# Kernel optimization log

Measured on AMD Instinct MI355X. Metric: run time of the kernel, lower is better.

The kernel has to match this reference:

```python
import jax, jax.numpy as jnp
import numpy as np

B, LQ, LK, D, NH = 16, 1024, 1024, 160, 8
HD = D // NH
EPS = 1e-5


def _ln(x, g, b):
    m = x.mean(-1, keepdims=True)
    v = ((x - m) ** 2).mean(-1, keepdims=True)
    return (x - m) / jnp.sqrt(v + EPS) * g + b


def _heads(x, L):
    # [B,L,D] -> [B,NH,L,HD]
    return x.reshape(B, L, NH, HD).transpose(0, 2, 1, 3)


def _attn(qh, kh, vh, scale):
    logits = jnp.einsum('bhqd,bhkd->bhqk', qh, kh) * scale
    p = jax.nn.softmax(logits, axis=-1)
    o = jnp.einsum('bhqk,bhkd->bhqd', p, vh)
    return o.transpose(0, 2, 1, 3).reshape(B, -1, D)


def setup_inputs() -> dict:
    key = jax.random.key(0)
    ks = jax.random.split(key, 16)
    s = 0.02
    inp = {
        'q': jax.random.normal(ks[0], (B, LQ, D), jnp.float32),
        'kv': jax.random.normal(ks[1], (B, LK, D), jnp.float32),
        'ln1_g': jnp.ones((D,), jnp.float32), 'ln1_b': jnp.zeros((D,), jnp.float32),
        'sa_in_w': jax.random.normal(ks[2], (3 * D, D), jnp.float32) * s,
        'sa_in_b': jnp.zeros((3 * D,), jnp.float32),
        'sa_out_w': jax.random.normal(ks[3], (D, D), jnp.float32) * s,
        'sa_out_b': jnp.zeros((D,), jnp.float32),
        'ln2_g': jnp.ones((D,), jnp.float32), 'ln2_b': jnp.zeros((D,), jnp.float32),
        'lnkv_g': jnp.ones((D,), jnp.float32), 'lnkv_b': jnp.zeros((D,), jnp.float32),
        'ca_qw': jax.random.normal(ks[4], (D, D), jnp.float32) * s,
        'ca_qb': jnp.zeros((D,), jnp.float32),
        'ca_kw': jax.random.normal(ks[5], (D, D), jnp.float32) * s,
        'ca_kb': jnp.zeros((D,), jnp.float32),
        'ca_vw': jax.random.normal(ks[6], (D, D), jnp.float32) * s,
        'ca_vb': jnp.zeros((D,), jnp.float32),
        'ca_ow': jax.random.normal(ks[7], (D, D), jnp.float32) * s,
        'ca_ob': jnp.zeros((D,), jnp.float32),
        'log_tau': jnp.zeros((1,), jnp.float32),
        'lnf_g': jnp.ones((D,), jnp.float32), 'lnf_b': jnp.zeros((D,), jnp.float32),
        'w1': jax.random.normal(ks[8], (4 * D, D), jnp.float32) * s,
        'b1': jnp.zeros((4 * D,), jnp.float32),
        'w2': jax.random.normal(ks[9], (D, 4 * D), jnp.float32) * s,
        'b2': jnp.zeros((D,), jnp.float32),
    }
    return inp


def reference(q, kv, ln1_g, ln1_b, sa_in_w, sa_in_b, sa_out_w, sa_out_b,
              ln2_g, ln2_b, lnkv_g, lnkv_b, ca_qw, ca_qb, ca_kw, ca_kb,
              ca_vw, ca_vb, ca_ow, ca_ob, log_tau, lnf_g, lnf_b,
              w1, b1, w2, b2):
    # --- self-attention (pre-LN), standard 1/sqrt(hd) scale ---
    qn = _ln(q, ln1_g, ln1_b)
    qkv = qn @ sa_in_w.T + sa_in_b  # [B,LQ,3D]
    sq, sk, sv = jnp.split(qkv, 3, axis=-1)
    sa = _attn(_heads(sq, LQ), _heads(sk, LQ), _heads(sv, LQ), HD ** -0.5)
    sa = sa @ sa_out_w.T + sa_out_b
    q = q + sa  # DropPath is identity in eval

    # --- cross-attention with learnable temperature ---
    qn = _ln(q, ln2_g, ln2_b)
    kvn = _ln(kv, lnkv_g, lnkv_b)
    tau = jnp.minimum(jax.nn.softplus(log_tau) + 0.5, 2.0)  # clamp max=2.0
    scale = (HD ** -0.5) / tau[0]
    qh = _heads(qn @ ca_qw.T + ca_qb, LQ)
    kh = _heads(kvn @ ca_kw.T + ca_kb, LK)
    vh = _heads(kvn @ ca_vw.T + ca_vb, LK)
    ca = _attn(qh, kh, vh, scale) @ ca_ow.T + ca_ob
    q = q + ca

    # --- FFN with exact GELU ---
    h = _ln(q, lnf_g, lnf_b) @ w1.T + b1
    h = jax.nn.gelu(h, approximate=False)
    q = q + (h @ w2.T + b2)
    return q
```

## Files before the change

### kernel.cpp

```cpp
#include <hip/hip_runtime.h>
#include <hip/hip_bf16.h>
#include <math.h>

#define LQN 1024
#define LKN 1024
#define NB 16
#define DM 160
#define NHEADS 8
#define HDIM 20

typedef __attribute__((ext_vector_type(8))) short bf16x8;
typedef __attribute__((ext_vector_type(4))) float f32x4;

__device__ __forceinline__ float bf2f(unsigned short h) {
  union { unsigned int u; float f; } c; c.u = ((unsigned int)h) << 16; return c.f;
}
__device__ __forceinline__ unsigned short f2bf(float f) {
  union { float f; unsigned int u; } c; c.f = f;
  unsigned int lsb = (c.u >> 16) & 1u;
  unsigned int r = c.u + 0x7fffu + lsb;
  return (unsigned short)(r >> 16);
}
__device__ __forceinline__ unsigned int cvtpk(float a, float b) {
  unsigned int r;
  asm("v_cvt_pk_bf16_f32 %0, %1, %2" : "=v"(r) : "v"(a), "v"(b));
  return r;
}
__device__ __forceinline__ float ex2(float x) { return __builtin_amdgcn_exp2f(x); }

struct CvtArgs {
  const float* src[8];
  int cum[9];
};

__global__ void init_kernel(uint4* __restrict__ zbase, int nz,
                            uint4* __restrict__ vbase, int nv,
                            const float* __restrict__ b0,
                            const float* __restrict__ b1,
                            const float* __restrict__ b2,
                            float* __restrict__ bcat,
                            CvtArgs a, unsigned short* __restrict__ wdst,
                            const float* __restrict__ x1,
                            const float* __restrict__ g1,
                            const float* __restrict__ bb1,
                            unsigned short* __restrict__ y1,
                            const float* __restrict__ x2,
                            const float* __restrict__ g2,
                            const float* __restrict__ bb2,
                            unsigned short* __restrict__ y2, int rowsPer) {
  int i = blockIdx.x * 256 + threadIdx.x;
  if (i < nz) zbase[i] = make_uint4(0, 0, 0, 0);
  if (i < nv) {
    unsigned int v = ((i & 31) == 20) ? 0x3F803F80u : 0u;
    vbase[i] = make_uint4(v, v, v, v);
  }
  if (i < 480) bcat[i] = (i < 160) ? b0[i] : (i < 320 ? b1[i - 160] : b2[i - 320]);
  if (i < 409600) {
    int s = 0;
#pragma unroll
    for (int t = 0; t < 7; ++t) s += (i >= a.cum[t + 1]) ? 1 : 0;
    wdst[i] = f2bf(a.src[s][i - a.cum[s]]);
  }
  int row = blockIdx.x * 4 + (threadIdx.x >> 6);
  int lane = threadIdx.x & 63;
  const float* x; const float* g; const float* b; unsigned short* y;
  if (row < rowsPer) {
    x = x1 + (size_t)row * DM; g = g1; b = bb1; y = y1 + (size_t)row * DM;
  } else {
    int r2 = row - rowsPer;
    x = x2 + (size_t)r2 * DM; g = g2; b = bb2; y = y2 + (size_t)r2 * DM;
  }
  float a0 = x[lane];
  float a1 = x[lane + 64];
  float a2 = (lane < 32) ? x[lane + 128] : 0.0f;
  float s = a0 + a1 + a2;
#pragma unroll
  for (int m = 1; m < 64; m <<= 1) s += __shfl_xor(s, m);
  float mean = s * (1.0f / DM);
  float d0 = a0 - mean, d1 = a1 - mean, d2 = a2 - mean;
  float vs = d0 * d0 + d1 * d1 + ((lane < 32) ? d2 * d2 : 0.0f);
#pragma unroll
  for (int m = 1; m < 64; m <<= 1) vs += __shfl_xor(vs, m);
  float rstd = rsqrtf(vs * (1.0f / DM) + 1e-5f);
  y[lane]      = f2bf(d0 * rstd * g[lane]      + b[lane]);
  y[lane + 64] = f2bf(d1 * rstd * g[lane + 64] + b[lane + 64]);
  if (lane < 32)
    y[lane + 128] = f2bf(d2 * rstd * g[lane + 128] + b[lane + 128]);
}

template <int EPI, int NCOL>
__global__ __launch_bounds__(256, 2)
void gemm160_kernel(const unsigned short* __restrict__ Aq,
                    const unsigned short* __restrict__ Akv,
                    const unsigned short* __restrict__ W,
                    const float* __restrict__ bias,
                    const float* __restrict__ res,
                    void* __restrict__ outp,
                    unsigned short* __restrict__ Kc,
                    unsigned short* __restrict__ Vc,
                    const float* __restrict__ lng,
                    const float* __restrict__ lnb) {
  __shared__ unsigned short wl[NCOL * 16 * 168];
  int tid = threadIdx.x;
  int lane = tid & 63;
  int w = tid >> 6;
  int y = blockIdx.y;
  const unsigned short* Wb = W + y * (NCOL * 2560);
  for (int idx = tid * 8; idx < NCOL * 2560; idx += 2048) {
    int col = idx / 160, k = idx % 160;
    *(uint4*)(wl + col * 168 + k) = *(const uint4*)(Wb + idx);
  }
  __syncthreads();
  int lr = lane & 15;
  int g = lane >> 4;
  int R0 = blockIdx.x * 64;
  int rbase = R0 + w * 16;
  const unsigned short* A = (EPI == 0 && y > 0) ? Akv : Aq;
  const unsigned short* Ap = A + (size_t)(rbase + lr) * 160 + g * 8;
  const unsigned short* wp = wl + lr * 168 + g * 8;
  f32x4 acc[NCOL];
#pragma unroll
  for (int c = 0; c < NCOL; ++c) acc[c] = (f32x4){0, 0, 0, 0};
#pragma unroll
  for (int k0 = 0; k0 < 160; k0 += 32) {
    bf16x8 a = *(const bf16x8*)(Ap + k0);
#pragma unroll
    for (int c = 0; c < NCOL; ++c) {
      bf16x8 bfr = *(const bf16x8*)(wp + c * 16 * 168 + k0);
      acc[c] = __builtin_amdgcn_mfma_f32_16x16x32_bf16(a, bfr, acc[c], 0, 0, 0);
    }
  }
  if (EPI == 0) {
    if (y == 0) {
      unsigned short* Qp = (unsigned short*)outp;
#pragma unroll
      for (int c = 0; c < NCOL; ++c) {
        int col = c * 16 + lr;
        int h = col / 20, d = col % 20;
        float bc = bias[col];
#pragma unroll
        for (int r = 0; r < 4; ++r) {
          int row = rbase + g * 4 + r;
          Qp[(size_t)row * 256 + h * 32 + d] = f2bf(acc[c][r] + bc);
        }
      }
    } else if (y == 1) {
      int b = R0 >> 10;
#pragma unroll
      for (int c = 0; c < NCOL; ++c) {
        int col = c * 16 + lr;
        int h = col / 20, d = col % 20;
        float bc = bias[160 + col];
        size_t base = ((((size_t)(b * 8 + h)) * 4 + (d >> 3)) * 1024) * 8 + (d & 7);
#pragma unroll
        for (int r = 0; r < 4; ++r) {
          int tok = (rbase + g * 4 + r) & 1023;
          Kc[base + (size_t)tok * 8] = f2bf(acc[c][r] + bc);
        }
      }
    } else {
      int b = R0 >> 10;
      int base64 = R0 & 1023;
      int slotbase = base64 + g * 8 + (w & 1) * 4 + (w >> 1) * 32;
#pragma unroll
      for (int c = 0; c < NCOL; ++c) {
        int col = c * 16 + lr;
        int h = col / 20, d = col % 20;
        float bc = bias[320 + col];
        size_t vb = ((size_t)(b * 8 + h) * 128) * 256 + (size_t)d * 8;
#pragma unroll
        for (int r = 0; r < 4; ++r) {
          int S = slotbase + r;
          Vc[vb + (size_t)(S >> 3) * 256 + (S & 7)] = f2bf(acc[c][r] + bc);
        }
      }
    }
  } else if (EPI == 2) {
    unsigned short* out = (unsigned short*)outp;
#pragma unroll
    for (int c = 0; c < NCOL; ++c) {
      int colg = y * NCOL * 16 + c * 16 + lr;
      float bc = bias[colg];
#pragma unroll
      for (int r = 0; r < 4; ++r) {
        int row = rbase + g * 4 + r;
        float v = acc[c][r] + bc;
        v = 0.5f * v * (1.0f + erff(v * 0.70710678118654752f));
        out[(size_t)row * 640 + colg] = f2bf(v);
      }
    }
  } else {
    float* out = (float*)outp;
#pragma unroll
    for (int c = 0; c < NCOL; ++c) {
      int col = c * 16 + lr;
      float bc = bias[col];
#pragma unroll
      for (int r = 0; r < 4; ++r) {
        int row = rbase + g * 4 + r;
        float v = acc[c][r] + bc + res[(size_t)row * 160 + col];
        acc[c][r] = v;
        out[(size_t)row * 160 + col] = v;
      }
    }
#pragma unroll
    for (int r = 0; r < 4; ++r) {
      float s = 0.0f, sq = 0.0f;
#pragma unroll
      for (int c = 0; c < NCOL; ++c) { s += acc[c][r]; sq += acc[c][r] * acc[c][r]; }
#pragma unroll
      for (int m = 1; m < 16; m <<= 1) { s += __shfl_xor(s, m); sq += __shfl_xor(sq, m); }
      float mean = s * (1.0f / DM);
      float var = sq * (1.0f / DM) - mean * mean;
      float rstd = rsqrtf(var + 1e-5f);
      int row = rbase + g * 4 + r;
#pragma unroll
      for (int c = 0; c < NCOL; ++c) {
        int col = c * 16 + lr;
        Kc[(size_t)row * 160 + col] =
            f2bf((acc[c][r] - mean) * rstd * lng[col] + lnb[col]);
      }
    }
  }
}

template <int K>
__global__ __launch_bounds__(256, 4)
void gemm_kernel(const unsigned short* __restrict__ A,
                 const unsigned short* __restrict__ W,
                 const float* __restrict__ bias,
                 const float* __restrict__ res,
                 float* __restrict__ out, int N) {
  int lane = threadIdx.x & 63;
  int wid = threadIdx.x >> 6;
  int wr = wid >> 1, wc = wid & 1;
  int r0 = blockIdx.x * 64 + wr * 32;
  int c0 = blockIdx.y * 64 + wc * 32;
  if (c0 >= N) return;
  int lr = lane & 15;
  int ko = (lane >> 4) * 8;
  const unsigned short* Ap0 = A + (size_t)(r0 + lr) * K + ko;
  const unsigned short* Ap1 = Ap0 + (size_t)16 * K;
  const unsigned short* Wp0 = W + (size_t)(c0 + lr) * K + ko;
  const unsigned short* Wp1 = Wp0 + (size_t)16 * K;
  f32x4 acc00 = {0, 0, 0, 0}, acc01 = {0, 0, 0, 0};
  f32x4 acc10 = {0, 0, 0, 0}, acc11 = {0, 0, 0, 0};
#pragma unroll
  for (int k = 0; k < K; k += 32) {
    bf16x8 a0 = *(const bf16x8*)(Ap0 + k);
    bf16x8 a1 = *(const bf16x8*)(Ap1 + k);
    bf16x8 b0 = *(const bf16x8*)(Wp0 + k);
    bf16x8 b1 = *(const bf16x8*)(Wp1 + k);
    acc00 = __builtin_amdgcn_mfma_f32_16x16x32_bf16(a0, b0, acc00, 0, 0, 0);
    acc01 = __builtin_amdgcn_mfma_f32_16x16x32_bf16(a0, b1, acc01, 0, 0, 0);
    acc10 = __builtin_amdgcn_mfma_f32_16x16x32_bf16(a1, b0, acc10, 0, 0, 0);
    acc11 = __builtin_amdgcn_mfma_f32_16x16x32_bf16(a1, b1, acc11, 0, 0, 0);
  }
  int cA = c0 + lr, cB = c0 + 16 + lr;
  float bc0 = bias[cA];
  float bc1 = bias[cB];
  int rb = (lane >> 4) * 4;
#pragma unroll
  for (int i = 0; i < 2; ++i) {
    f32x4 aA = i ? acc10 : acc00;
    f32x4 aB = i ? acc11 : acc01;
#pragma unroll
    for (int r = 0; r < 4; ++r) {
      int row = r0 + i * 16 + rb + r;
      out[(size_t)row * N + cA] = aA[r] + bc0 + res[(size_t)row * N + cA];
      out[(size_t)row * N + cB] = aB[r] + bc1 + res[(size_t)row * N + cB];
    }
  }
}

__global__ __launch_bounds__(256, 4)
void attn_kernel(const unsigned short* __restrict__ Qp,
                 const unsigned short* __restrict__ Kc,
                 const unsigned short* __restrict__ Vc,
                 unsigned short* __restrict__ O,
                 const float* __restrict__ tau_ptr,
                 float base_scale) {
  __shared__ unsigned short kbuf[2][4096];
  __shared__ unsigned short vbuf[2][4096];
  int lane = threadIdx.x & 63;
  int wid = threadIdx.x >> 6;
  int bh = blockIdx.x;
  int b = bh >> 3, h = bh & 7;
  int q0 = blockIdx.y * 128 + wid * 32;
  float sc = base_scale;
  if (tau_ptr) {
    float lt = tau_ptr[0];
    float sp = (lt > 20.0f) ? lt : log1pf(expf(lt));
    sc /= fminf(sp + 0.5f, 2.0f);
  }
  float scale = sc * 1.4426950408889634f;
  int lr = lane & 15;
  int g = lane >> 4;
  int ko = g * 8;
  int rb = g * 4;
  const size_t tb = (size_t)b * LQN;
  union { bf16x8 v; unsigned short s[8]; unsigned int u[4]; } fq0, fq1;
  fq0.v = *(const bf16x8*)(Qp + (tb + q0 + lr) * 256 + h * 32 + ko);
  fq1.v = *(const bf16x8*)(Qp + (tb + q0 + 16 + lr) * 256 + h * 32 + ko);
#pragma unroll
  for (int j = 0; j < 4; ++j) {
    fq0.u[j] = cvtpk(bf2f(fq0.s[2 * j]) * scale, bf2f(fq0.s[2 * j + 1]) * scale);
    fq1.u[j] = cvtpk(bf2f(fq1.s[2 * j]) * scale, bf2f(fq1.s[2 * j + 1]) * scale);
  }
  bf16x8 aq0 = fq0.v, aq1 = fq1.v;
  const unsigned short* ksrc = Kc + (((size_t)bh * 4 + wid) * 1024) * 8;
  const unsigned short* vsrc = Vc + (size_t)bh * 32768;
  int sd = wid * 1024 + lane * 8;
  {
    uint4 k0 = *(const uint4*)(ksrc + lane * 8);
    uint4 k1 = *(const uint4*)(ksrc + (64 + lane) * 8);
    uint4 v0 = *(const uint4*)(vsrc + sd);
    uint4 v1 = *(const uint4*)(vsrc + sd + 512);
    *(uint4*)(kbuf[0] + sd) = k0;
    *(uint4*)(kbuf[0] + sd + 512) = k1;
    *(uint4*)(vbuf[0] + sd) = v0;
    *(uint4*)(vbuf[0] + sd + 512) = v1;
  }
  __syncthreads();
  int cur = 0;
  f32x4 o00 = {0, 0, 0, 0}, o01 = {0, 0, 0, 0};
  f32x4 o10 = {0, 0, 0, 0}, o11 = {0, 0, 0, 0};
  const f32x4 zero = {0, 0, 0, 0};

#define ATTN_COMPUTE(KB, VB)                                                   \
  {                                                                            \
    const unsigned short* kp_ = (KB);                                          \
    const unsigned short* vp_ = (VB);                                          \
    bf16x8 ck0 = *(const bf16x8*)(kp_ + g * 1024 + lr * 8);                    \
    bf16x8 ck1 = *(const bf16x8*)(kp_ + g * 1024 + (16 + lr) * 8);             \
    bf16x8 ck2 = *(const bf16x8*)(kp_ + g * 1024 + (32 + lr) * 8);             \
    bf16x8 ck3 = *(const bf16x8*)(kp_ + g * 1024 + (48 + lr) * 8);             \
    __builtin_amdgcn_s_setprio(1);                                             \
    f32x4 s0 = __builtin_amdgcn_mfma_f32_16x16x32_bf16(ck0, aq0, zero, 0, 0, 0);\
    f32x4 s1 = __builtin_amdgcn_mfma_f32_16x16x32_bf16(ck1, aq0, zero, 0, 0, 0);\
    f32x4 s2 = __builtin_amdgcn_mfma_f32_16x16x32_bf16(ck2, aq0, zero, 0, 0, 0);\
    f32x4 s3 = __builtin_amdgcn_mfma_f32_16x16x32_bf16(ck3, aq0, zero, 0, 0, 0);\
    __builtin_amdgcn_s_setprio(0);                                             \
    union { bf16x8 v; unsigned int u[4]; } p1, p2, p3, p4;                     \
    p1.u[0] = cvtpk(ex2(s0[0]), ex2(s0[1]));                                   \
    p1.u[1] = cvtpk(ex2(s0[2]), ex2(s0[3]));                                   \
    p1.u[2] = cvtpk(ex2(s1[0]), ex2(s1[1]));                                   \
    p1.u[3] = cvtpk(ex2(s1[2]), ex2(s1[3]));                                   \
    p2.u[0] = cvtpk(ex2(s2[0]), ex2(s2[1]));                                   \
    p2.u[1] = cvtpk(ex2(s2[2]), ex2(s2[3]));                                   \
    p2.u[2] = cvtpk(ex2(s3[0]), ex2(s3[1]));                                   \
    p2.u[3] = cvtpk(ex2(s3[2]), ex2(s3[3]));                                   \
    __builtin_amdgcn_s_setprio(1);                                             \
    s0 = __builtin_amdgcn_mfma_f32_16x16x32_bf16(ck0, aq1, zero, 0, 0, 0);     \
    s1 = __builtin_amdgcn_mfma_f32_16x16x32_bf16(ck1, aq1, zero, 0, 0, 0);     \
    s2 = __builtin_amdgcn_mfma_f32_16x16x32_bf16(ck2, aq1, zero, 0, 0, 0);     \
    s3 = __builtin_amdgcn_mfma_f32_16x16x32_bf16(ck3, aq1, zero, 0, 0, 0);     \
    __builtin_amdgcn_s_setprio(0);                                             \
    p3.u[0] = cvtpk(ex2(s0[0]), ex2(s0[1]));                                   \
    p3.u[1] = cvtpk(ex2(s0[2]), ex2(s0[3]));                                   \
    p3.u[2] = cvtpk(ex2(s1[0]), ex2(s1[1]));                                   \
    p3.u[3] = cvtpk(ex2(s1[2]), ex2(s1[3]));                                   \
    p4.u[0] = cvtpk(ex2(s2[0]), ex2(s2[1]));                                   \
    p4.u[1] = cvtpk(ex2(s2[2]), ex2(s2[3]));                                   \
    p4.u[2] = cvtpk(ex2(s3[0]), ex2(s3[1]));                                   \
    p4.u[3] = cvtpk(ex2(s3[2]), ex2(s3[3]));                                   \
    bf16x8 w00 = *(const bf16x8*)(vp_ + g * 256 + lr * 8);                     \
    bf16x8 w01 = *(const bf16x8*)(vp_ + (4 + g) * 256 + lr * 8);               \
    bf16x8 w10 = *(const bf16x8*)(vp_ + g * 256 + (16 + lr) * 8);              \
    bf16x8 w11 = *(const bf16x8*)(vp_ + (4 + g) * 256 + (16 + lr) * 8);        \
    __builtin_amdgcn_s_setprio(1);                                             \
    o00 = __builtin_amdgcn_mfma_f32_16x16x32_bf16(p1.v, w00, o00, 0, 0, 0);    \
    o00 = __builtin_amdgcn_mfma_f32_16x16x32_bf16(p2.v, w01, o00, 0, 0, 0);    \
    o01 = __builtin_amdgcn_mfma_f32_16x16x32_bf16(p1.v, w10, o01, 0, 0, 0);    \
    o01 = __builtin_amdgcn_mfma_f32_16x16x32_bf16(p2.v, w11, o01, 0, 0, 0);    \
    o10 = __builtin_amdgcn_mfma_f32_16x16x32_bf16(p3.v, w00, o10, 0, 0, 0);    \
    o10 = __builtin_amdgcn_mfma_f32_16x16x32_bf16(p4.v, w01, o10, 0, 0, 0);    \
    o11 = __builtin_amdgcn_mfma_f32_16x16x32_bf16(p3.v, w10, o11, 0, 0, 0);    \
    o11 = __builtin_amdgcn_mfma_f32_16x16x32_bf16(p4.v, w11, o11, 0, 0, 0);    \
    __builtin_amdgcn_s_setprio(0);                                             \
  }

#pragma unroll 1
  for (int kt = 0; kt < LKN; kt += 128) {
    int ktn = (kt + 128 < LKN) ? kt + 128 : 0;
    uint4 kA0 = *(const uint4*)(ksrc + (ktn + lane) * 8);
    uint4 kA1 = *(const uint4*)(ksrc + (ktn + 64 + lane) * 8);
    uint4 vA0 = *(const uint4*)(vsrc + ktn * 32 + sd);
    uint4 vA1 = *(const uint4*)(vsrc + ktn * 32 + sd + 512);
    ATTN_COMPUTE(kbuf[cur], vbuf[cur])
    *(uint4*)(kbuf[cur ^ 1] + sd) = kA0;
    *(uint4*)(kbuf[cur ^ 1] + sd + 512) = kA1;
    ATTN_COMPUTE(kbuf[cur] + 512, vbuf[cur] + 2048)
    *(uint4*)(vbuf[cur ^ 1] + sd) = vA0;
    *(uint4*)(vbuf[cur ^ 1] + sd + 512) = vA1;
    __syncthreads();
    cur ^= 1;
  }
#undef ATTN_COMPUTE
  unsigned short* ob = O + (tb + q0) * DM + h * HDIM;
  int psl = (lane & 48) + 4;
#pragma unroll
  for (int r = 0; r < 4; ++r) {
    int qr = rb + r;
    float inv0 = 1.0f / __shfl(o01[r], psl, 64);
    ob[(size_t)qr * DM + lr] = f2bf(o00[r] * inv0);
    if (lr < 4) ob[(size_t)qr * DM + 16 + lr] = f2bf(o01[r] * inv0);
    float inv1 = 1.0f / __shfl(o11[r], psl, 64);
    ob[(size_t)(16 + qr) * DM + lr] = f2bf(o10[r] * inv1);
    if (lr < 4) ob[(size_t)(16 + qr) * DM + 16 + lr] = f2bf(o11[r] * inv1);
  }
}

extern "C" void kernel_launch(void* const* d_in, const int* in_sizes, int n_in,
                              void* d_out, int out_size, void* d_ws, size_t ws_size,
                              hipStream_t stream) {
  (void)in_sizes; (void)n_in; (void)out_size; (void)ws_size;
  const float* q        = (const float*)d_in[0];
  const float* kv       = (const float*)d_in[1];
  const float* ln1_g    = (const float*)d_in[2];
  const float* ln1_b    = (const float*)d_in[3];
  const float* sa_in_w  = (const float*)d_in[4];
  const float* sa_in_b  = (const float*)d_in[5];
  const float* sa_out_w = (const float*)d_in[6];
  const float* sa_out_b = (const float*)d_in[7];
  const float* ln2_g    = (const float*)d_in[8];
  const float* ln2_b    = (const float*)d_in[9];
  const float* lnkv_g   = (const float*)d_in[10];
  const float* lnkv_b   = (const float*)d_in[11];
  const float* ca_qw    = (const float*)d_in[12];
  const float* ca_qb    = (const float*)d_in[13];
  const float* ca_kw    = (const float*)d_in[14];
  const float* ca_kb    = (const float*)d_in[15];
  const float* ca_vw    = (const float*)d_in[16];
  const float* ca_vb    = (const float*)d_in[17];
  const float* ca_ow    = (const float*)d_in[18];
  const float* ca_ob    = (const float*)d_in[19];
  const float* log_tau  = (const float*)d_in[20];
  const float* lnf_g    = (const float*)d_in[21];
  const float* lnf_b    = (const float*)d_in[22];
  const float* w1       = (const float*)d_in[23];
  const float* b1       = (const float*)d_in[24];
  const float* w2       = (const float*)d_in[25];
  const float* b2       = (const float*)d_in[26];

  const int M = NB * LQN;
  char* ws = (char*)d_ws;
  unsigned short* wb   = (unsigned short*)(ws);
  float*          bcat = (float*)(ws + 860160);
  unsigned short* qn   = (unsigned short*)(ws + 1048576);
  unsigned short* sqp  = (unsigned short*)(ws + 6291456);
  unsigned short* skc  = (unsigned short*)(ws + 14680064);
  unsigned short* svc  = (unsigned short*)(ws + 23068672);
  unsigned short* attn = (unsigned short*)(ws + 31457280);
  unsigned short* kvn  = (unsigned short*)(ws + 36700160);
  float*          q1   = (float*)(ws + 41943040);
  float*          q2   = (float*)(ws + 52428800);
  unsigned short* hbuf = (unsigned short*)(ws + 6291456);

  unsigned short* b_sa_in  = wb;
  unsigned short* b_sa_out = wb + 76800;
  unsigned short* b_ca_q   = wb + 102400;
  unsigned short* b_ca_o   = wb + 179200;
  unsigned short* b_w1     = wb + 204800;
  unsigned short* b_w2     = wb + 307200;

  dim3 blk(256);
  const float isq = 0.22360679774997896f;

  CvtArgs ca;
  ca.src[0] = sa_in_w;  ca.src[1] = sa_out_w; ca.src[2] = ca_qw; ca.src[3] = ca_kw;
  ca.src[4] = ca_vw;    ca.src[5] = ca_ow;    ca.src[6] = w1;    ca.src[7] = w2;
  int cum[9] = {0, 76800, 102400, 128000, 153600, 179200, 204800, 307200, 409600};
  for (int i = 0; i < 9; ++i) ca.cum[i] = cum[i];
  init_kernel<<<dim3(M / 2), blk, 0, stream>>>(
      (uint4*)(ws + 6291456), 1048576, (uint4*)(ws + 23068672), 524288,
      ca_qb, ca_kb, ca_vb, bcat, ca, wb,
      q, ln1_g, ln1_b, qn, kv, lnkv_g, lnkv_b, kvn, M);

  gemm160_kernel<0, 10><<<dim3(M / 64, 3), blk, 0, stream>>>(
      qn, qn, b_sa_in, sa_in_b, nullptr, sqp, skc, svc, nullptr, nullptr);
  attn_kernel<<<dim3(NB * NHEADS, LQN / 128), blk, 0, stream>>>(sqp, skc, svc, attn, nullptr, isq);
  gemm160_kernel<3, 10><<<dim3(M / 64, 1), blk, 0, stream>>>(
      attn, attn, b_sa_out, sa_out_b, q, q1, qn, nullptr, ln2_g, ln2_b);

  gemm160_kernel<0, 10><<<dim3(M / 64, 3), blk, 0, stream>>>(
      qn, kvn, b_ca_q, bcat, nullptr, sqp, skc, svc, nullptr, nullptr);
  attn_kernel<<<dim3(NB * NHEADS, LQN / 128), blk, 0, stream>>>(sqp, skc, svc, attn, log_tau, isq);
  gemm160_kernel<3, 10><<<dim3(M / 64, 1), blk, 0, stream>>>(
      attn, attn, b_ca_o, ca_ob, q1, q2, qn, nullptr, lnf_g, lnf_b);

  gemm160_kernel<2, 10><<<dim3(M / 64, 4), blk, 0, stream>>>(
      qn, qn, b_w1, b1, nullptr, hbuf, nullptr, nullptr, nullptr, nullptr);
  gemm_kernel<640><<<dim3(M / 64, 3), blk, 0, stream>>>(hbuf, b_w2, b2, q2, (float*)d_out, 160);
}
```

Baseline: 163.8 us.

## Give each wave private K/V LDS tiles to drop block-wide barriers

The attention kernel no longer shares double-buffered K/V tiles across the four waves of a block. Each wave now loads its own copy of every 64-key tile from global memory into a private LDS region, with the next tile prefetched into registers while the current one is computed. This removes the per-iteration __syncthreads so waves can run independently. The cost is four times the global/L2 load traffic per block, twice as many loop iterations, and reliance on in-order LDS access within a wave for the single-buffer overwrite.

```diff
diff --git a/kernel.cpp b/kernel.cpp
--- a/kernel.cpp
+++ b/kernel.cpp
@@ -280,8 +280,8 @@
                  unsigned short* __restrict__ O,
                  const float* __restrict__ tau_ptr,
                  float base_scale) {
-  __shared__ unsigned short kbuf[2][4096];
-  __shared__ unsigned short vbuf[2][4096];
+  __shared__ unsigned short kpriv[4][2048];
+  __shared__ unsigned short vpriv[4][2048];
   int lane = threadIdx.x & 63;
   int wid = threadIdx.x >> 6;
   int bh = blockIdx.x;
@@ -308,95 +308,97 @@
     fq1.u[j] = cvtpk(bf2f(fq1.s[2 * j]) * scale, bf2f(fq1.s[2 * j + 1]) * scale);
   }
   bf16x8 aq0 = fq0.v, aq1 = fq1.v;
-  const unsigned short* ksrc = Kc + (((size_t)bh * 4 + wid) * 1024) * 8;
+  const unsigned short* ksrc = Kc + (size_t)bh * 32768;
   const unsigned short* vsrc = Vc + (size_t)bh * 32768;
-  int sd = wid * 1024 + lane * 8;
-  {
-    uint4 k0 = *(const uint4*)(ksrc + lane * 8);
-    uint4 k1 = *(const uint4*)(ksrc + (64 + lane) * 8);
-    uint4 v0 = *(const uint4*)(vsrc + sd);
-    uint4 v1 = *(const uint4*)(vsrc + sd + 512);
-    *(uint4*)(kbuf[0] + sd) = k0;
-    *(uint4*)(kbuf[0] + sd + 512) = k1;
-    *(uint4*)(vbuf[0] + sd) = v0;
-    *(uint4*)(vbuf[0] + sd + 512) = v1;
-  }
-  __syncthreads();
-  int cur = 0;
+  unsigned short* kw = kpriv[wid];
+  unsigned short* vw = vpriv[wid];
+  int lo = lane * 8;
+  uint4 kr0 = *(const uint4*)(ksrc + lo);
+  uint4 kr1 = *(const uint4*)(ksrc + 8192 + lo);
+  uint4 kr2 = *(const uint4*)(ksrc + 16384 + lo);
+  uint4 kr3 = *(const uint4*)(ksrc + 24576 + lo);
+  uint4 vr0 = *(const uint4*)(vsrc + lo);
+  uint4 vr1 = *(const uint4*)(vsrc + 512 + lo);
+  uint4 vr2 = *(const uint4*)(vsrc + 1024 + lo);
+  uint4 vr3 = *(const uint4*)(vsrc + 1536 + lo);
+  *(uint4*)(kw + lo) = kr0;
+  *(uint4*)(kw + 512 + lo) = kr1;
+  *(uint4*)(kw + 1024 + lo) = kr2;
+  *(uint4*)(kw + 1536 + lo) = kr3;
+  *(uint4*)(vw + lo) = vr0;
+  *(uint4*)(vw + 512 + lo) = vr1;
+  *(uint4*)(vw + 1024 + lo) = vr2;
+  *(uint4*)(vw + 1536 + lo) = vr3;
   f32x4 o00 = {0, 0, 0, 0}, o01 = {0, 0, 0, 0};
   f32x4 o10 = {0, 0, 0, 0}, o11 = {0, 0, 0, 0};
   const f32x4 zero = {0, 0, 0, 0};
-
-#define ATTN_COMPUTE(KB, VB)                                                   \
-  {                                                                            \
-    const unsigned short* kp_ = (KB);                                          \
-    const unsigned short* vp_ = (VB);                                          \
-    bf16x8 ck0 = *(const bf16x8*)(kp_ + g * 1024 + lr * 8);                    \
-    bf16x8 ck1 = *(const bf16x8*)(kp_ + g * 1024 + (16 + lr) * 8);             \
-    bf16x8 ck2 = *(const bf16x8*)(kp_ + g * 1024 + (32 + lr) * 8);             \
-    bf16x8 ck3 = *(const bf16x8*)(kp_ + g * 1024 + (48 + lr) * 8);             \
-    __builtin_amdgcn_s_setprio(1);                                             \
-    f32x4 s0 = __builtin_amdgcn_mfma_f32_16x16x32_bf16(ck0, aq0, zero, 0, 0, 0);\
-    f32x4 s1 = __builtin_amdgcn_mfma_f32_16x16x32_bf16(ck1, aq0, zero, 0, 0, 0);\
-    f32x4 s2 = __builtin_amdgcn_mfma_f32_16x16x32_bf16(ck2, aq0, zero, 0, 0, 0);\
-    f32x4 s3 = __builtin_amdgcn_mfma_f32_16x16x32_bf16(ck3, aq0, zero, 0, 0, 0);\
-    __builtin_amdgcn_s_setprio(0);                                             \
-    union { bf16x8 v; unsigned int u[4]; } p1, p2, p3, p4;                     \
-    p1.u[0] = cvtpk(ex2(s0[0]), ex2(s0[1]));                                   \
-    p1.u[1] = cvtpk(ex2(s0[2]), ex2(s0[3]));                                   \
-    p1.u[2] = cvtpk(ex2(s1[0]), ex2(s1[1]));                                   \
-    p1.u[3] = cvtpk(ex2(s1[2]), ex2(s1[3]));                                   \
-    p2.u[0] = cvtpk(ex2(s2[0]), ex2(s2[1]));                                   \
-    p2.u[1] = cvtpk(ex2(s2[2]), ex2(s2[3]));                                   \
-    p2.u[2] = cvtpk(ex2(s3[0]), ex2(s3[1]));                                   \
-    p2.u[3] = cvtpk(ex2(s3[2]), ex2(s3[3]));                                   \
-    __builtin_amdgcn_s_setprio(1);                                             \
-    s0 = __builtin_amdgcn_mfma_f32_16x16x32_bf16(ck0, aq1, zero, 0, 0, 0);     \
-    s1 = __builtin_amdgcn_mfma_f32_16x16x32_bf16(ck1, aq1, zero, 0, 0, 0);     \
-    s2 = __builtin_amdgcn_mfma_f32_16x16x32_bf16(ck2, aq1, zero, 0, 0, 0);     \
-    s3 = __builtin_amdgcn_mfma_f32_16x16x32_bf16(ck3, aq1, zero, 0, 0, 0);     \
-    __builtin_amdgcn_s_setprio(0);                                             \
-    p3.u[0] = cvtpk(ex2(s0[0]), ex2(s0[1]));                                   \
-    p3.u[1] = cvtpk(ex2(s0[2]), ex2(s0[3]));                                   \
-    p3.u[2] = cvtpk(ex2(s1[0]), ex2(s1[1]));                                   \
-    p3.u[3] = cvtpk(ex2(s1[2]), ex2(s1[3]));                                   \
-    p4.u[0] = cvtpk(ex2(s2[0]), ex2(s2[1]));                                   \
-    p4.u[1] = cvtpk(ex2(s2[2]), ex2(s2[3]));                                   \
-    p4.u[2] = cvtpk(ex2(s3[0]), ex2(s3[1]));                                   \
-    p4.u[3] = cvtpk(ex2(s3[2]), ex2(s3[3]));                                   \
-    bf16x8 w00 = *(const bf16x8*)(vp_ + g * 256 + lr * 8);                     \
-    bf16x8 w01 = *(const bf16x8*)(vp_ + (4 + g) * 256 + lr * 8);               \
-    bf16x8 w10 = *(const bf16x8*)(vp_ + g * 256 + (16 + lr) * 8);              \
-    bf16x8 w11 = *(const bf16x8*)(vp_ + (4 + g) * 256 + (16 + lr) * 8);        \
-    __builtin_amdgcn_s_setprio(1);                                             \
-    o00 = __builtin_amdgcn_mfma_f32_16x16x32_bf16(p1.v, w00, o00, 0, 0, 0);    \
-    o00 = __builtin_amdgcn_mfma_f32_16x16x32_bf16(p2.v, w01, o00, 0, 0, 0);    \
-    o01 = __builtin_amdgcn_mfma_f32_16x16x32_bf16(p1.v, w10, o01, 0, 0, 0);    \
-    o01 = __builtin_amdgcn_mfma_f32_16x16x32_bf16(p2.v, w11, o01, 0, 0, 0);    \
-    o10 = __builtin_amdgcn_mfma_f32_16x16x32_bf16(p3.v, w00, o10, 0, 0, 0);    \
-    o10 = __builtin_amdgcn_mfma_f32_16x16x32_bf16(p4.v, w01, o10, 0, 0, 0);    \
-    o11 = __builtin_amdgcn_mfma_f32_16x16x32_bf16(p3.v, w10, o11, 0, 0, 0);    \
-    o11 = __builtin_amdgcn_mfma_f32_16x16x32_bf16(p4.v, w11, o11, 0, 0, 0);    \
-    __builtin_amdgcn_s_setprio(0);                                             \
-  }
-
 #pragma unroll 1
-  for (int kt = 0; kt < LKN; kt += 128) {
-    int ktn = (kt + 128 < LKN) ? kt + 128 : 0;
-    uint4 kA0 = *(const uint4*)(ksrc + (ktn + lane) * 8);
-    uint4 kA1 = *(const uint4*)(ksrc + (ktn + 64 + lane) * 8);
-    uint4 vA0 = *(const uint4*)(vsrc + ktn * 32 + sd);
-    uint4 vA1 = *(const uint4*)(vsrc + ktn * 32 + sd + 512);
-    ATTN_COMPUTE(kbuf[cur], vbuf[cur])
-    *(uint4*)(kbuf[cur ^ 1] + sd) = kA0;
-    *(uint4*)(kbuf[cur ^ 1] + sd + 512) = kA1;
-    ATTN_COMPUTE(kbuf[cur] + 512, vbuf[cur] + 2048)
-    *(uint4*)(vbuf[cur ^ 1] + sd) = vA0;
-    *(uint4*)(vbuf[cur ^ 1] + sd + 512) = vA1;
-    __syncthreads();
-    cur ^= 1;
-  }
-#undef ATTN_COMPUTE
+  for (int kt = 0; kt < LKN; kt += 64) {
+    int ktn = (kt + 64 < LKN) ? kt + 64 : 0;
+    kr0 = *(const uint4*)(ksrc + ktn * 8 + lo);
+    kr1 = *(const uint4*)(ksrc + 8192 + ktn * 8 + lo);
+    kr2 = *(const uint4*)(ksrc + 16384 + ktn * 8 + lo);
+    kr3 = *(const uint4*)(ksrc + 24576 + ktn * 8 + lo);
+    vr0 = *(const uint4*)(vsrc + ktn * 32 + lo);
+    vr1 = *(const uint4*)(vsrc + ktn * 32 + 512 + lo);
+    vr2 = *(const uint4*)(vsrc + ktn * 32 + 1024 + lo);
+    vr3 = *(const uint4*)(vsrc + ktn * 32 + 1536 + lo);
+    bf16x8 ck0 = *(const bf16x8*)(kw + g * 512 + lr * 8);
+    bf16x8 ck1 = *(const bf16x8*)(kw + g * 512 + (16 + lr) * 8);
+    bf16x8 ck2 = *(const bf16x8*)(kw + g * 512 + (32 + lr) * 8);
+    bf16x8 ck3 = *(const bf16x8*)(kw + g * 512 + (48 + lr) * 8);
+    __builtin_amdgcn_s_setprio(1);
+    f32x4 s0 = __builtin_amdgcn_mfma_f32_16x16x32_bf16(ck0, aq0, zero, 0, 0, 0);
+    f32x4 s1 = __builtin_amdgcn_mfma_f32_16x16x32_bf16(ck1, aq0, zero, 0, 0, 0);
+    f32x4 s2 = __builtin_amdgcn_mfma_f32_16x16x32_bf16(ck2, aq0, zero, 0, 0, 0);
+    f32x4 s3 = __builtin_amdgcn_mfma_f32_16x16x32_bf16(ck3, aq0, zero, 0, 0, 0);
+    __builtin_amdgcn_s_setprio(0);
+    union { bf16x8 v; unsigned int u[4]; } p1, p2, p3, p4;
+    p1.u[0] = cvtpk(ex2(s0[0]), ex2(s0[1]));
+    p1.u[1] = cvtpk(ex2(s0[2]), ex2(s0[3]));
+    p1.u[2] = cvtpk(ex2(s1[0]), ex2(s1[1]));
+    p1.u[3] = cvtpk(ex2(s1[2]), ex2(s1[3]));
+    p2.u[0] = cvtpk(ex2(s2[0]), ex2(s2[1]));
+    p2.u[1] = cvtpk(ex2(s2[2]), ex2(s2[3]));
+    p2.u[2] = cvtpk(ex2(s3[0]), ex2(s3[1]));
+    p2.u[3] = cvtpk(ex2(s3[2]), ex2(s3[3]));
+    __builtin_amdgcn_s_setprio(1);
+    s0 = __builtin_amdgcn_mfma_f32_16x16x32_bf16(ck0, aq1, zero, 0, 0, 0);
+    s1 = __builtin_amdgcn_mfma_f32_16x16x32_bf16(ck1, aq1, zero, 0, 0, 0);
+    s2 = __builtin_amdgcn_mfma_f32_16x16x32_bf16(ck2, aq1, zero, 0, 0, 0);
+    s3 = __builtin_amdgcn_mfma_f32_16x16x32_bf16(ck3, aq1, zero, 0, 0, 0);
+    __builtin_amdgcn_s_setprio(0);
+    p3.u[0] = cvtpk(ex2(s0[0]), ex2(s0[1]));
+    p3.u[1] = cvtpk(ex2(s0[2]), ex2(s0[3]));
+    p3.u[2] = cvtpk(ex2(s1[0]), ex2(s1[1]));
+    p3.u[3] = cvtpk(ex2(s1[2]), ex2(s1[3]));
+    p4.u[0] = cvtpk(ex2(s2[0]), ex2(s2[1]));
+    p4.u[1] = cvtpk(ex2(s2[2]), ex2(s2[3]));
+    p4.u[2] = cvtpk(ex2(s3[0]), ex2(s3[1]));
+    p4.u[3] = cvtpk(ex2(s3[2]), ex2(s3[3]));
+    bf16x8 w00 = *(const bf16x8*)(vw + g * 256 + lr * 8);
+    bf16x8 w01 = *(const bf16x8*)(vw + (4 + g) * 256 + lr * 8);
+    bf16x8 w10 = *(const bf16x8*)(vw + g * 256 + (16 + lr) * 8);
+    bf16x8 w11 = *(const bf16x8*)(vw + (4 + g) * 256 + (16 + lr) * 8);
+    __builtin_amdgcn_s_setprio(1);
+    o00 = __builtin_amdgcn_mfma_f32_16x16x32_bf16(p1.v, w00, o00, 0, 0, 0);
+    o00 = __builtin_amdgcn_mfma_f32_16x16x32_bf16(p2.v, w01, o00, 0, 0, 0);
+    o01 = __builtin_amdgcn_mfma_f32_16x16x32_bf16(p1.v, w10, o01, 0, 0, 0);
+    o01 = __builtin_amdgcn_mfma_f32_16x16x32_bf16(p2.v, w11, o01, 0, 0, 0);
+    o10 = __builtin_amdgcn_mfma_f32_16x16x32_bf16(p3.v, w00, o10, 0, 0, 0);
+    o10 = __builtin_amdgcn_mfma_f32_16x16x32_bf16(p4.v, w01, o10, 0, 0, 0);
+    o11 = __builtin_amdgcn_mfma_f32_16x16x32_bf16(p3.v, w10, o11, 0, 0, 0);
+    o11 = __builtin_amdgcn_mfma_f32_16x16x32_bf16(p4.v, w11, o11, 0, 0, 0);
+    __builtin_amdgcn_s_setprio(0);
+    *(uint4*)(kw + lo) = kr0;
+    *(uint4*)(kw + 512 + lo) = kr1;
+    *(uint4*)(kw + 1024 + lo) = kr2;
+    *(uint4*)(kw + 1536 + lo) = kr3;
+    *(uint4*)(vw + lo) = vr0;
+    *(uint4*)(vw + 512 + lo) = vr1;
+    *(uint4*)(vw + 1024 + lo) = vr2;
+    *(uint4*)(vw + 1536 + lo) = vr3;
+  }
   unsigned short* ob = O + (tb + q0) * DM + h * HDIM;
   int psl = (lane & 48) + 4;
 #pragma unroll
```

New measurement: 173.0 us. 1.06x slower.

## Fuse FFN up-projection, GELU and down-projection into one kernel

Applied to the files above, without the earlier changes.

Replaces the separate W1+GELU GEMM and the W2 GEMM with a single kernel that processes the 640-wide hidden dimension in four 160-wide chunks. Each chunk's weights are staged into LDS and the GELU output is kept in per-wave LDS, then consumed immediately by the down-projection. This removes the global write and read of the 16K x 640 bf16 hidden buffer and one launch. In exchange it uses large LDS (~190KB) with one block per CU, reloads both weight chunks per block with syncs, and issues fewer wavefronts.

```diff
diff --git a/kernel.cpp b/kernel.cpp
--- a/kernel.cpp
+++ b/kernel.cpp
@@ -175,20 +175,6 @@
         }
       }
     }
-  } else if (EPI == 2) {
-    unsigned short* out = (unsigned short*)outp;
-#pragma unroll
-    for (int c = 0; c < NCOL; ++c) {
-      int colg = y * NCOL * 16 + c * 16 + lr;
-      float bc = bias[colg];
-#pragma unroll
-      for (int r = 0; r < 4; ++r) {
-        int row = rbase + g * 4 + r;
-        float v = acc[c][r] + bc;
-        v = 0.5f * v * (1.0f + erff(v * 0.70710678118654752f));
-        out[(size_t)row * 640 + colg] = f2bf(v);
-      }
-    }
   } else {
     float* out = (float*)outp;
 #pragma unroll
@@ -224,51 +210,85 @@
   }
 }
 
-template <int K>
-__global__ __launch_bounds__(256, 4)
-void gemm_kernel(const unsigned short* __restrict__ A,
-                 const unsigned short* __restrict__ W,
-                 const float* __restrict__ bias,
-                 const float* __restrict__ res,
-                 float* __restrict__ out, int N) {
-  int lane = threadIdx.x & 63;
-  int wid = threadIdx.x >> 6;
-  int wr = wid >> 1, wc = wid & 1;
-  int r0 = blockIdx.x * 64 + wr * 32;
-  int c0 = blockIdx.y * 64 + wc * 32;
-  if (c0 >= N) return;
+__global__ __launch_bounds__(256, 1)
+void ffn_kernel(const unsigned short* __restrict__ A,
+                const unsigned short* __restrict__ W1,
+                const float* __restrict__ B1,
+                const unsigned short* __restrict__ W2,
+                const float* __restrict__ B2,
+                const float* __restrict__ res,
+                float* __restrict__ out) {
+  __shared__ unsigned short w1l[160 * 168];
+  __shared__ unsigned short w2l[160 * 168];
+  __shared__ unsigned short hl[4][16 * 168];
+  int tid = threadIdx.x;
+  int lane = tid & 63;
+  int w = tid >> 6;
   int lr = lane & 15;
-  int ko = (lane >> 4) * 8;
-  const unsigned short* Ap0 = A + (size_t)(r0 + lr) * K + ko;
-  const unsigned short* Ap1 = Ap0 + (size_t)16 * K;
-  const unsigned short* Wp0 = W + (size_t)(c0 + lr) * K + ko;
-  const unsigned short* Wp1 = Wp0 + (size_t)16 * K;
-  f32x4 acc00 = {0, 0, 0, 0}, acc01 = {0, 0, 0, 0};
-  f32x4 acc10 = {0, 0, 0, 0}, acc11 = {0, 0, 0, 0};
-#pragma unroll
-  for (int k = 0; k < K; k += 32) {
-    bf16x8 a0 = *(const bf16x8*)(Ap0 + k);
-    bf16x8 a1 = *(const bf16x8*)(Ap1 + k);
-    bf16x8 b0 = *(const bf16x8*)(Wp0 + k);
-    bf16x8 b1 = *(const bf16x8*)(Wp1 + k);
-    acc00 = __builtin_amdgcn_mfma_f32_16x16x32_bf16(a0, b0, acc00, 0, 0, 0);
-    acc01 = __builtin_amdgcn_mfma_f32_16x16x32_bf16(a0, b1, acc01, 0, 0, 0);
-    acc10 = __builtin_amdgcn_mfma_f32_16x16x32_bf16(a1, b0, acc10, 0, 0, 0);
-    acc11 = __builtin_amdgcn_mfma_f32_16x16x32_bf16(a1, b1, acc11, 0, 0, 0);
-  }
-  int cA = c0 + lr, cB = c0 + 16 + lr;
-  float bc0 = bias[cA];
-  float bc1 = bias[cB];
-  int rb = (lane >> 4) * 4;
-#pragma unroll
-  for (int i = 0; i < 2; ++i) {
-    f32x4 aA = i ? acc10 : acc00;
-    f32x4 aB = i ? acc11 : acc01;
+  int g = lane >> 4;
+  int rbase = blockIdx.x * 64 + w * 16;
+  const unsigned short* Ap = A + (size_t)(rbase + lr) * 160 + g * 8;
+  unsigned short* hw = hl[w];
+  const unsigned short* hrd = hw + lr * 168 + g * 8;
+  f32x4 acc2[10];
+#pragma unroll
+  for (int c = 0; c < 10; ++c) acc2[c] = (f32x4){0, 0, 0, 0};
+#pragma unroll 1
+  for (int j = 0; j < 4; ++j) {
+    __syncthreads();
+    const unsigned short* W1b = W1 + j * 25600;
+    for (int idx = tid * 8; idx < 25600; idx += 2048) {
+      int col = idx / 160, k = idx % 160;
+      *(uint4*)(w1l + col * 168 + k) = *(const uint4*)(W1b + idx);
+    }
+    for (int idx = tid * 8; idx < 25600; idx += 2048) {
+      int o = idx / 160, k = idx % 160;
+      *(uint4*)(w2l + o * 168 + k) = *(const uint4*)(W2 + (size_t)o * 640 + j * 160 + k);
+    }
+    __syncthreads();
+    f32x4 acc1[10];
+#pragma unroll
+    for (int c = 0; c < 10; ++c) acc1[c] = (f32x4){0, 0, 0, 0};
+    const unsigned short* wp = w1l + lr * 168 + g * 8;
+#pragma unroll
+    for (int k0 = 0; k0 < 160; k0 += 32) {
+      bf16x8 a = *(const bf16x8*)(Ap + k0);
+#pragma unroll
+      for (int c = 0; c < 10; ++c) {
+        bf16x8 bfr = *(const bf16x8*)(wp + c * 16 * 168 + k0);
+        acc1[c] = __builtin_amdgcn_mfma_f32_16x16x32_bf16(a, bfr, acc1[c], 0, 0, 0);
+      }
+    }
+#pragma unroll
+    for (int c = 0; c < 10; ++c) {
+      int col = c * 16 + lr;
+      float bc = B1[j * 160 + col];
+#pragma unroll
+      for (int r = 0; r < 4; ++r) {
+        float v = acc1[c][r] + bc;
+        v = 0.5f * v * (1.0f + erff(v * 0.70710678118654752f));
+        hw[(g * 4 + r) * 168 + col] = f2bf(v);
+      }
+    }
+    const unsigned short* w2p = w2l + lr * 168 + g * 8;
+#pragma unroll
+    for (int k0 = 0; k0 < 160; k0 += 32) {
+      bf16x8 a2 = *(const bf16x8*)(hrd + k0);
+#pragma unroll
+      for (int c = 0; c < 10; ++c) {
+        bf16x8 b2f = *(const bf16x8*)(w2p + c * 16 * 168 + k0);
+        acc2[c] = __builtin_amdgcn_mfma_f32_16x16x32_bf16(a2, b2f, acc2[c], 0, 0, 0);
+      }
+    }
+  }
+#pragma unroll
+  for (int c = 0; c < 10; ++c) {
+    int col = c * 16 + lr;
+    float bc = B2[col];
 #pragma unroll
     for (int r = 0; r < 4; ++r) {
-      int row = r0 + i * 16 + rb + r;
-      out[(size_t)row * N + cA] = aA[r] + bc0 + res[(size_t)row * N + cA];
-      out[(size_t)row * N + cB] = aB[r] + bc1 + res[(size_t)row * N + cB];
+      int row = rbase + g * 4 + r;
+      out[(size_t)row * 160 + col] = acc2[c][r] + bc + res[(size_t)row * 160 + col];
     }
   }
 }
@@ -455,7 +475,6 @@
   unsigned short* kvn  = (unsigned short*)(ws + 36700160);
   float*          q1   = (float*)(ws + 41943040);
   float*          q2   = (float*)(ws + 52428800);
-  unsigned short* hbuf = (unsigned short*)(ws + 6291456);
 
   unsigned short* b_sa_in  = wb;
   unsigned short* b_sa_out = wb + 76800;
@@ -489,7 +508,6 @@
   gemm160_kernel<3, 10><<<dim3(M / 64, 1), blk, 0, stream>>>(
       attn, attn, b_ca_o, ca_ob, q1, q2, qn, nullptr, lnf_g, lnf_b);
 
-  gemm160_kernel<2, 10><<<dim3(M / 64, 4), blk, 0, stream>>>(
-      qn, qn, b_w1, b1, nullptr, hbuf, nullptr, nullptr, nullptr, nullptr);
-  gemm_kernel<640><<<dim3(M / 64, 3), blk, 0, stream>>>(hbuf, b_w2, b2, q2, (float*)d_out, 160);
-}
+  ffn_kernel<<<dim3(M / 64), blk, 0, stream>>>(
+      qn, b_w1, b1, b_w2, b2, q2, (float*)d_out);
+}
```

New measurement: 171.5 us. 4.7% more time.

## Process 64 query rows per wave in attention to reuse K/V fragments

Applied to the files above, without the earlier changes.

Each attention wave now handles 64 query rows instead of 32, so each block covers 256 queries and the grid along the query axis is halved. The K and V fragments loaded from shared memory are reused across four query sub-tiles, which halves LDS reads and global K/V tile loads per query. The cost is more accumulator and Q registers per thread, a lower occupancy hint (launch bounds 2 instead of 4), and fewer blocks (512) to spread across the GPU.

```diff
diff --git a/kernel.cpp b/kernel.cpp
--- a/kernel.cpp
+++ b/kernel.cpp
@@ -273,7 +273,7 @@
   }
 }
 
-__global__ __launch_bounds__(256, 4)
+__global__ __launch_bounds__(256, 2)
 void attn_kernel(const unsigned short* __restrict__ Qp,
                  const unsigned short* __restrict__ Kc,
                  const unsigned short* __restrict__ Vc,
@@ -286,7 +286,7 @@
   int wid = threadIdx.x >> 6;
   int bh = blockIdx.x;
   int b = bh >> 3, h = bh & 7;
-  int q0 = blockIdx.y * 128 + wid * 32;
+  int q0 = blockIdx.y * 256 + wid * 64;
   float sc = base_scale;
   if (tau_ptr) {
     float lt = tau_ptr[0];
@@ -299,15 +299,19 @@
   int ko = g * 8;
   int rb = g * 4;
   const size_t tb = (size_t)b * LQN;
-  union { bf16x8 v; unsigned short s[8]; unsigned int u[4]; } fq0, fq1;
+  union { bf16x8 v; unsigned short s[8]; unsigned int u[4]; } fq0, fq1, fq2, fq3;
   fq0.v = *(const bf16x8*)(Qp + (tb + q0 + lr) * 256 + h * 32 + ko);
   fq1.v = *(const bf16x8*)(Qp + (tb + q0 + 16 + lr) * 256 + h * 32 + ko);
+  fq2.v = *(const bf16x8*)(Qp + (tb + q0 + 32 + lr) * 256 + h * 32 + ko);
+  fq3.v = *(const bf16x8*)(Qp + (tb + q0 + 48 + lr) * 256 + h * 32 + ko);
 #pragma unroll
   for (int j = 0; j < 4; ++j) {
     fq0.u[j] = cvtpk(bf2f(fq0.s[2 * j]) * scale, bf2f(fq0.s[2 * j + 1]) * scale);
     fq1.u[j] = cvtpk(bf2f(fq1.s[2 * j]) * scale, bf2f(fq1.s[2 * j + 1]) * scale);
-  }
-  bf16x8 aq0 = fq0.v, aq1 = fq1.v;
+    fq2.u[j] = cvtpk(bf2f(fq2.s[2 * j]) * scale, bf2f(fq2.s[2 * j + 1]) * scale);
+    fq3.u[j] = cvtpk(bf2f(fq3.s[2 * j]) * scale, bf2f(fq3.s[2 * j + 1]) * scale);
+  }
+  bf16x8 aq0 = fq0.v, aq1 = fq1.v, aq2 = fq2.v, aq3 = fq3.v;
   const unsigned short* ksrc = Kc + (((size_t)bh * 4 + wid) * 1024) * 8;
   const unsigned short* vsrc = Vc + (size_t)bh * 32768;
   int sd = wid * 1024 + lane * 8;
@@ -325,21 +329,17 @@
   int cur = 0;
   f32x4 o00 = {0, 0, 0, 0}, o01 = {0, 0, 0, 0};
   f32x4 o10 = {0, 0, 0, 0}, o11 = {0, 0, 0, 0};
+  f32x4 o20 = {0, 0, 0, 0}, o21 = {0, 0, 0, 0};
+  f32x4 o30 = {0, 0, 0, 0}, o31 = {0, 0, 0, 0};
   const f32x4 zero = {0, 0, 0, 0};
 
-#define ATTN_COMPUTE(KB, VB)                                                   \
+#define QPASS(AQA, AQB, OA0, OA1, OB0, OB1)                                    \
   {                                                                            \
-    const unsigned short* kp_ = (KB);                                          \
-    const unsigned short* vp_ = (VB);                                          \
-    bf16x8 ck0 = *(const bf16x8*)(kp_ + g * 1024 + lr * 8);                    \
-    bf16x8 ck1 = *(const bf16x8*)(kp_ + g * 1024 + (16 + lr) * 8);             \
-    bf16x8 ck2 = *(const bf16x8*)(kp_ + g * 1024 + (32 + lr) * 8);             \
-    bf16x8 ck3 = *(const bf16x8*)(kp_ + g * 1024 + (48 + lr) * 8);             \
     __builtin_amdgcn_s_setprio(1);                                             \
-    f32x4 s0 = __builtin_amdgcn_mfma_f32_16x16x32_bf16(ck0, aq0, zero, 0, 0, 0);\
-    f32x4 s1 = __builtin_amdgcn_mfma_f32_16x16x32_bf16(ck1, aq0, zero, 0, 0, 0);\
-    f32x4 s2 = __builtin_amdgcn_mfma_f32_16x16x32_bf16(ck2, aq0, zero, 0, 0, 0);\
-    f32x4 s3 = __builtin_amdgcn_mfma_f32_16x16x32_bf16(ck3, aq0, zero, 0, 0, 0);\
+    f32x4 s0 = __builtin_amdgcn_mfma_f32_16x16x32_bf16(ck0, AQA, zero, 0, 0, 0);\
+    f32x4 s1 = __builtin_amdgcn_mfma_f32_16x16x32_bf16(ck1, AQA, zero, 0, 0, 0);\
+    f32x4 s2 = __builtin_amdgcn_mfma_f32_16x16x32_bf16(ck2, AQA, zero, 0, 0, 0);\
+    f32x4 s3 = __builtin_amdgcn_mfma_f32_16x16x32_bf16(ck3, AQA, zero, 0, 0, 0);\
     __builtin_amdgcn_s_setprio(0);                                             \
     union { bf16x8 v; unsigned int u[4]; } p1, p2, p3, p4;                     \
     p1.u[0] = cvtpk(ex2(s0[0]), ex2(s0[1]));                                   \
@@ -351,10 +351,10 @@
     p2.u[2] = cvtpk(ex2(s3[0]), ex2(s3[1]));                                   \
     p2.u[3] = cvtpk(ex2(s3[2]), ex2(s3[3]));                                   \
     __builtin_amdgcn_s_setprio(1);                                             \
-    s0 = __builtin_amdgcn_mfma_f32_16x16x32_bf16(ck0, aq1, zero, 0, 0, 0);     \
-    s1 = __builtin_amdgcn_mfma_f32_16x16x32_bf16(ck1, aq1, zero, 0, 0, 0);     \
-    s2 = __builtin_amdgcn_mfma_f32_16x16x32_bf16(ck2, aq1, zero, 0, 0, 0);     \
-    s3 = __builtin_amdgcn_mfma_f32_16x16x32_bf16(ck3, aq1, zero, 0, 0, 0);     \
+    s0 = __builtin_amdgcn_mfma_f32_16x16x32_bf16(ck0, AQB, zero, 0, 0, 0);     \
+    s1 = __builtin_amdgcn_mfma_f32_16x16x32_bf16(ck1, AQB, zero, 0, 0, 0);     \
+    s2 = __builtin_amdgcn_mfma_f32_16x16x32_bf16(ck2, AQB, zero, 0, 0, 0);     \
+    s3 = __builtin_amdgcn_mfma_f32_16x16x32_bf16(ck3, AQB, zero, 0, 0, 0);     \
     __builtin_amdgcn_s_setprio(0);                                             \
     p3.u[0] = cvtpk(ex2(s0[0]), ex2(s0[1]));                                   \
     p3.u[1] = cvtpk(ex2(s0[2]), ex2(s0[3]));                                   \
@@ -364,20 +364,32 @@
     p4.u[1] = cvtpk(ex2(s2[2]), ex2(s2[3]));                                   \
     p4.u[2] = cvtpk(ex2(s3[0]), ex2(s3[1]));                                   \
     p4.u[3] = cvtpk(ex2(s3[2]), ex2(s3[3]));                                   \
+    __builtin_amdgcn_s_setprio(1);                                             \
+    OA0 = __builtin_amdgcn_mfma_f32_16x16x32_bf16(p1.v, w00, OA0, 0, 0, 0);    \
+    OA0 = __builtin_amdgcn_mfma_f32_16x16x32_bf16(p2.v, w01, OA0, 0, 0, 0);    \
+    OA1 = __builtin_amdgcn_mfma_f32_16x16x32_bf16(p1.v, w10, OA1, 0, 0, 0);    \
+    OA1 = __builtin_amdgcn_mfma_f32_16x16x32_bf16(p2.v, w11, OA1, 0, 0, 0);    \
+    OB0 = __builtin_amdgcn_mfma_f32_16x16x32_bf16(p3.v, w00, OB0, 0, 0, 0);    \
+    OB0 = __builtin_amdgcn_mfma_f32_16x16x32_bf16(p4.v, w01, OB0, 0, 0, 0);    \
+    OB1 = __builtin_amdgcn_mfma_f32_16x16x32_bf16(p3.v, w10, OB1, 0, 0, 0);    \
+    OB1 = __builtin_amdgcn_mfma_f32_16x16x32_bf16(p4.v, w11, OB1, 0, 0, 0);    \
+    __builtin_amdgcn_s_setprio(0);                                             \
+  }
+
+#define ATTN_COMPUTE(KB, VB)                                                   \
+  {                                                                            \
+    const unsigned short* kp_ = (KB);                                          \
+    const unsigned short* vp_ = (VB);                                          \
+    bf16x8 ck0 = *(const bf16x8*)(kp_ + g * 1024 + lr * 8);                    \
+    bf16x8 ck1 = *(const bf16x8*)(kp_ + g * 1024 + (16 + lr) * 8);             \
+    bf16x8 ck2 = *(const bf16x8*)(kp_ + g * 1024 + (32 + lr) * 8);             \
+    bf16x8 ck3 = *(const bf16x8*)(kp_ + g * 1024 + (48 + lr) * 8);             \
     bf16x8 w00 = *(const bf16x8*)(vp_ + g * 256 + lr * 8);                     \
     bf16x8 w01 = *(const bf16x8*)(vp_ + (4 + g) * 256 + lr * 8);               \
     bf16x8 w10 = *(const bf16x8*)(vp_ + g * 256 + (16 + lr) * 8);              \
     bf16x8 w11 = *(const bf16x8*)(vp_ + (4 + g) * 256 + (16 + lr) * 8);        \
-    __builtin_amdgcn_s_setprio(1);                                             \
-    o00 = __builtin_amdgcn_mfma_f32_16x16x32_bf16(p1.v, w00, o00, 0, 0, 0);    \
-    o00 = __builtin_amdgcn_mfma_f32_16x16x32_bf16(p2.v, w01, o00, 0, 0, 0);    \
-    o01 = __builtin_amdgcn_mfma_f32_16x16x32_bf16(p1.v, w10, o01, 0, 0, 0);    \
-    o01 = __builtin_amdgcn_mfma_f32_16x16x32_bf16(p2.v, w11, o01, 0, 0, 0);    \
-    o10 = __builtin_amdgcn_mfma_f32_16x16x32_bf16(p3.v, w00, o10, 0, 0, 0);    \
-    o10 = __builtin_amdgcn_mfma_f32_16x16x32_bf16(p4.v, w01, o10, 0, 0, 0);    \
-    o11 = __builtin_amdgcn_mfma_f32_16x16x32_bf16(p3.v, w10, o11, 0, 0, 0);    \
-    o11 = __builtin_amdgcn_mfma_f32_16x16x32_bf16(p4.v, w11, o11, 0, 0, 0);    \
-    __builtin_amdgcn_s_setprio(0);                                             \
+    QPASS(aq0, aq1, o00, o01, o10, o11)                                        \
+    QPASS(aq2, aq3, o20, o21, o30, o31)                                        \
   }
 
 #pragma unroll 1
@@ -397,6 +409,7 @@
     cur ^= 1;
   }
 #undef ATTN_COMPUTE
+#undef QPASS
   unsigned short* ob = O + (tb + q0) * DM + h * HDIM;
   int psl = (lane & 48) + 4;
 #pragma unroll
@@ -408,6 +421,12 @@
     float inv1 = 1.0f / __shfl(o11[r], psl, 64);
     ob[(size_t)(16 + qr) * DM + lr] = f2bf(o10[r] * inv1);
     if (lr < 4) ob[(size_t)(16 + qr) * DM + 16 + lr] = f2bf(o11[r] * inv1);
+    float inv2 = 1.0f / __shfl(o21[r], psl, 64);
+    ob[(size_t)(32 + qr) * DM + lr] = f2bf(o20[r] * inv2);
+    if (lr < 4) ob[(size_t)(32 + qr) * DM + 16 + lr] = f2bf(o21[r] * inv2);
+    float inv3 = 1.0f / __shfl(o31[r], psl, 64);
+    ob[(size_t)(48 + qr) * DM + lr] = f2bf(o30[r] * inv3);
+    if (lr < 4) ob[(size_t)(48 + qr) * DM + 16 + lr] = f2bf(o31[r] * inv3);
   }
 }
 
@@ -479,13 +498,13 @@
 
   gemm160_kernel<0, 10><<<dim3(M / 64, 3), blk, 0, stream>>>(
       qn, qn, b_sa_in, sa_in_b, nullptr, sqp, skc, svc, nullptr, nullptr);
-  attn_kernel<<<dim3(NB * NHEADS, LQN / 128), blk, 0, stream>>>(sqp, skc, svc, attn, nullptr, isq);
+  attn_kernel<<<dim3(NB * NHEADS, LQN / 256), blk, 0, stream>>>(sqp, skc, svc, attn, nullptr, isq);
   gemm160_kernel<3, 10><<<dim3(M / 64, 1), blk, 0, stream>>>(
       attn, attn, b_sa_out, sa_out_b, q, q1, qn, nullptr, ln2_g, ln2_b);
 
   gemm160_kernel<0, 10><<<dim3(M / 64, 3), blk, 0, stream>>>(
       qn, kvn, b_ca_q, bcat, nullptr, sqp, skc, svc, nullptr, nullptr);
-  attn_kernel<<<dim3(NB * NHEADS, LQN / 128), blk, 0, stream>>>(sqp, skc, svc, attn, log_tau, isq);
+  attn_kernel<<<dim3(NB * NHEADS, LQN / 256), blk, 0, stream>>>(sqp, skc, svc, attn, log_tau, isq);
   gemm160_kernel<3, 10><<<dim3(M / 64, 1), blk, 0, stream>>>(
       attn, attn, b_ca_o, ca_ob, q1, q2, qn, nullptr, lnf_g, lnf_b);
 
```

Result: no change. 164.3 us (+0.3%).
